# Performance work log

Measured on AMD Instinct MI355X. Metric: run time of the kernel, lower is better.

## Reference

```python
import jax, jax.numpy as jnp
import numpy as np

B, N, H = 2, 4096, 1024
HEADS, DHEAD, M = 16, 64, 256
KERNEL_EPS = 1e-3


def setup_inputs() -> dict:
    key = jax.random.key(0)
    ks = jax.random.split(key, 10)
    w = lambda k, shp: jax.random.normal(k, shp, dtype=jnp.float32) * 0.02
    return {
        "hidden_states": jax.random.normal(ks[0], (B, N, H), dtype=jnp.float32),
        "Wq": w(ks[1], (H, H)), "bq": jnp.zeros((H,), jnp.float32),
        "Wk": w(ks[2], (H, H)), "bk": jnp.zeros((H,), jnp.float32),
        "Wv": w(ks[3], (H, H)), "bv": jnp.zeros((H,), jnp.float32),
        "Wo": w(ks[4], (H, H)), "bo": jnp.zeros((H,), jnp.float32),
        "proj": jax.random.normal(ks[5], (M, DHEAD), dtype=jnp.float32),
    }


def _split_heads(x):
    b, n, _ = x.shape
    return x.reshape(b, n, HEADS, DHEAD).transpose(0, 2, 1, 3)  # [b,h,n,d]


def _softmax_kernel(data, proj, is_query):
    # data: [b,h,n,d]; proj: [m,d]
    data_normalizer = DHEAD ** (-0.25)
    data_dash = jnp.einsum('bhnd,md->bhnm', data_normalizer * data, proj)
    diag_data = -0.5 * jnp.sum(data * data, axis=-1, keepdims=True)  # [b,h,n,1]
    if is_query:
        # argmax over a size-1 last dim -> stabilizer == diag_data itself
        stab = diag_data
    else:
        stab = jnp.max(diag_data)
    kernel_out = jnp.exp(diag_data + (data_dash - stab))  # exp kernel: exp(h + x)
    return (M ** (-0.5)) * (kernel_out + KERNEL_EPS)


def _performer_forward(hidden_states, Wq, bq, Wk, bk, Wv, bv, Wo, bo, proj):
    q = _split_heads(jnp.einsum('bni,oi->bno', hidden_states, Wq) + bq)
    k = _split_heads(jnp.einsum('bni,oi->bno', hidden_states, Wk) + bk)
    v = _split_heads(jnp.einsum('bni,oi->bno', hidden_states, Wv) + bv)

    qf = _softmax_kernel(q, proj, is_query=True)   # [b,h,n,m]
    kf = _softmax_kernel(k, proj, is_query=False)  # [b,h,n,m]

    # linear_attention (non-causal FAVOR+)
    k_cumsum = kf.sum(axis=-2)                                   # [b,h,m]
    d_inv = 1.0 / jnp.einsum('bhnm,bhm->bhn', qf, k_cumsum)      # [b,h,n]
    context = jnp.einsum('bhnm,bhne->bhme', kf, v)               # [b,h,m,d]
    out = jnp.einsum('bhme,bhnm,bhn->bhne', context, qf, d_inv)  # [b,h,n,d]

    out = out.transpose(0, 2, 1, 3).reshape(hidden_states.shape[0], -1, H)
    return jnp.einsum('bni,oi->bno', out, Wo) + bo


def reference(hidden_states, Wq, bq, Wk, bk, Wv, bv, Wo, bo, proj):
    return _performer_forward(hidden_states, Wq, bq, Wk, bk, Wv, bv, Wo, bo, proj)
```

## Files before the change

kernel.cpp:

```cpp
#include <hip/hip_runtime.h>
#include <math.h>

#define B_      2
#define N_      4096
#define H_      1024
#define HEADS_  16
#define DH_     64
#define M_      256
#define NSPLIT  8
#define EPAD    80

constexpr float NORMALIZER = 0.35355339059327373f;
constexpr float RATIO      = 0.0625f;
constexpr float KEPS       = 1e-3f;

typedef __bf16 bf16x8 __attribute__((ext_vector_type(8)));
typedef __bf16 bf16x4 __attribute__((ext_vector_type(4)));
typedef float  f32x4  __attribute__((ext_vector_type(4)));

__global__ __launch_bounds__(256) void split_bf16(
    const float* __restrict__ src, __bf16* __restrict__ hi, __bf16* __restrict__ lo)
{
    int i = blockIdx.x * 256 + threadIdx.x;
    float4 v = ((const float4*)src)[i];
    float vv[4] = {v.x, v.y, v.z, v.w};
    bf16x4 h, l;
#pragma unroll
    for (int j = 0; j < 4; ++j) {
        __bf16 hh = (__bf16)vv[j];
        h[j] = hh;
        l[j] = (__bf16)(vv[j] - (float)hh);
    }
    ((bf16x4*)hi)[i] = h;
    ((bf16x4*)lo)[i] = l;
}

__global__ __launch_bounds__(256) void split_w(
    const float* __restrict__ W0, const float* __restrict__ W1,
    const float* __restrict__ W2, const float* __restrict__ W3,
    __bf16* __restrict__ hi, __bf16* __restrict__ lo)
{
    const float* src = W0;
    if (blockIdx.y == 1) src = W1;
    else if (blockIdx.y == 2) src = W2;
    else if (blockIdx.y == 3) src = W3;
    int i = blockIdx.x * 256 + threadIdx.x;
    size_t o = (size_t)blockIdx.y * 262144 + i;
    float4 v = ((const float4*)src)[i];
    float vv[4] = {v.x, v.y, v.z, v.w};
    bf16x4 h, l;
#pragma unroll
    for (int j = 0; j < 4; ++j) {
        __bf16 hh = (__bf16)vv[j];
        h[j] = hh;
        l[j] = (__bf16)(vv[j] - (float)hh);
    }
    ((bf16x4*)hi)[o] = h;
    ((bf16x4*)lo)[o] = l;
}

__global__ __launch_bounds__(512, 2) void gemm_qkv(
    const __bf16* __restrict__ Ah, const __bf16* __restrict__ Al,
    const __bf16* __restrict__ WH, const __bf16* __restrict__ WL,
    const float* __restrict__ bq, const float* __restrict__ bk, const float* __restrict__ bv,
    __bf16* __restrict__ Qh, __bf16* __restrict__ Ql,
    __bf16* __restrict__ Kh, __bf16* __restrict__ Kl,
    __bf16* __restrict__ Vh, __bf16* __restrict__ Vl)
{
    __shared__ alignas(16) __bf16 lds[2][8][128 * 32];

    const int t    = threadIdx.x;
    const int lane = t & 63;
    const int lm   = lane & 15;
    const int lq   = lane >> 4;
    const int w    = t >> 6;
    const int wm   = (w >> 2) * 64;
    const int wn   = (w & 3) * 32;

    const int wg = blockIdx.x + 8 * blockIdx.y;
    const int sw = (wg & 7) * 64 + (wg >> 3);
    const int n0 = (sw & 7) * 128;
    const int m0 = (sw >> 3) * 128;
    const int K  = 1024;
    const int NK = 32;
    const size_t WSZ = (size_t)H_ * H_;

    const __bf16* mysrc;
    if      (w == 0) mysrc = Ah;
    else if (w == 1) mysrc = Al;
    else             mysrc = ((w & 1) ? WL : WH) + (size_t)((w - 2) >> 1) * WSZ;
    const int rbase  = (w < 2) ? m0 : n0;
    const int rsub   = lane >> 2;
    const int slot   = lane & 3;
    const int schunk = slot ^ ((lane >> 3) & 3);
    const __bf16* gbase = mysrc + (size_t)(rbase + rsub) * K + schunk * 8;

    f32x4 acc[3][4][2];
#pragma unroll
    for (int s = 0; s < 3; ++s)
#pragma unroll
        for (int i = 0; i < 4; ++i)
#pragma unroll
            for (int j = 0; j < 2; ++j) acc[s][i][j] = (f32x4){0.f, 0.f, 0.f, 0.f};

    const int swz = (lq ^ ((lm >> 1) & 3)) * 8;

    auto stage = [&](int buf, int k0) {
#pragma unroll
        for (int c = 0; c < 8; ++c) {
            const __bf16* g = gbase + (size_t)c * 16 * K + k0;
            __builtin_amdgcn_global_load_lds(
                (const __attribute__((address_space(1))) void*)g,
                (__attribute__((address_space(3))) void*)&lds[buf][w][c * 512],
                16, 0, 0);
        }
    };

#define MFMA_S(S) \
    _Pragma("unroll") \
    for (int i = 0; i < 4; ++i) \
        _Pragma("unroll") \
        for (int j = 0; j < 2; ++j) { \
            acc[S][i][j] = __builtin_amdgcn_mfma_f32_16x16x32_bf16(ah[i], bh[j], acc[S][i][j], 0, 0, 0); \
            acc[S][i][j] = __builtin_amdgcn_mfma_f32_16x16x32_bf16(al[i], bh[j], acc[S][i][j], 0, 0, 0); \
            acc[S][i][j] = __builtin_amdgcn_mfma_f32_16x16x32_bf16(ah[i], bl[j], acc[S][i][j], 0, 0, 0); \
        }

    stage(0, 0);
    int p = 0;
#pragma unroll 1
    for (int kt = 0; kt < NK; ++kt) {
        const int nb  = p ^ 1;
        const int nk0 = (kt + 1) * 32;
        const bool more = (kt < NK - 1);
        bf16x8 ah[4], al[4], bh[2], bl[2];

        if (w < 4) asm volatile("s_waitcnt vmcnt(0)" ::: "memory");
        asm volatile("s_barrier" ::: "memory");
#pragma unroll
        for (int i = 0; i < 4; ++i) {
            int off = (wm + i * 16 + lm) * 32 + swz;
            ah[i] = *(const bf16x8*)&lds[p][0][off];
            al[i] = *(const bf16x8*)&lds[p][1][off];
        }
#pragma unroll
        for (int j = 0; j < 2; ++j) {
            int off = (wn + j * 16 + lm) * 32 + swz;
            bh[j] = *(const bf16x8*)&lds[p][2][off];
            bl[j] = *(const bf16x8*)&lds[p][3][off];
        }
        if (more && w < 4) stage(nb, nk0);
        asm volatile("s_waitcnt lgkmcnt(0)" ::: "memory");
        __builtin_amdgcn_sched_barrier(0);
        __builtin_amdgcn_s_setprio(1);
        MFMA_S(0)
        __builtin_amdgcn_s_setprio(0);

        if (w == 4 || w == 5) asm volatile("s_waitcnt vmcnt(0)" ::: "memory");
        asm volatile("s_barrier" ::: "memory");
#pragma unroll
        for (int j = 0; j < 2; ++j) {
            int off = (wn + j * 16 + lm) * 32 + swz;
            bh[j] = *(const bf16x8*)&lds[p][4][off];
            bl[j] = *(const bf16x8*)&lds[p][5][off];
        }
        if (more && (w == 4 || w == 5)) stage(nb, nk0);
        asm volatile("s_waitcnt lgkmcnt(0)" ::: "memory");
        __builtin_amdgcn_sched_barrier(0);
        __builtin_amdgcn_s_setprio(1);
        MFMA_S(1)
        __builtin_amdgcn_s_setprio(0);

        if (w >= 6) asm volatile("s_waitcnt vmcnt(0)" ::: "memory");
        asm volatile("s_barrier" ::: "memory");
#pragma unroll
        for (int j = 0; j < 2; ++j) {
            int off = (wn + j * 16 + lm) * 32 + swz;
            bh[j] = *(const bf16x8*)&lds[p][6][off];
            bl[j] = *(const bf16x8*)&lds[p][7][off];
        }
        if (more && w >= 6) stage(nb, nk0);
        asm volatile("s_waitcnt lgkmcnt(0)" ::: "memory");
        __builtin_amdgcn_sched_barrier(0);
        __builtin_amdgcn_s_setprio(1);
        MFMA_S(2)
        __builtin_amdgcn_s_setprio(0);

        p ^= 1;
    }
#undef MFMA_S

    const float* biases[3] = {bq, bk, bv};
    __bf16* Chs[3] = {Qh, Kh, Vh};
    __bf16* Cls[3] = {Ql, Kl, Vl};
#pragma unroll
    for (int s = 0; s < 3; ++s) {
        float bsr[2];
#pragma unroll
        for (int j = 0; j < 2; ++j) bsr[j] = biases[s][n0 + wn + j * 16 + lm];
#pragma unroll
        for (int i = 0; i < 4; ++i)
#pragma unroll
            for (int r = 0; r < 4; ++r) {
                int rowm = m0 + wm + i * 16 + lq * 4 + r;
#pragma unroll
                for (int j = 0; j < 2; ++j) {
                    int col = n0 + wn + j * 16 + lm;
                    float o = acc[s][i][j][r] + bsr[j];
                    __bf16 hh = (__bf16)o;
                    Chs[s][(size_t)rowm * 1024 + col] = hh;
                    Cls[s][(size_t)rowm * 1024 + col] = (__bf16)(o - (float)hh);
                }
            }
    }
}

__global__ __launch_bounds__(512, 4) void gemm_out(
    const __bf16* __restrict__ Ah, const __bf16* __restrict__ Al,
    const __bf16* __restrict__ Bh, const __bf16* __restrict__ Bl,
    const float* __restrict__ bias, float* __restrict__ C0)
{
    __shared__ alignas(16) __bf16 lds[2][4][128 * 32];

    const int t    = threadIdx.x;
    const int lane = t & 63;
    const int lm   = lane & 15;
    const int lq   = lane >> 4;
    const int w    = t >> 6;
    const int wm   = (w >> 2) * 64;
    const int wn   = (w & 3) * 32;

    const int wg = blockIdx.x + 8 * blockIdx.y;
    const int sw = (wg & 7) * 64 + (wg >> 3);
    const int n0 = (sw & 7) * 128;
    const int m0 = (sw >> 3) * 128;
    const int K  = 1024;
    const int NK = 32;

    const int tw = w >> 1;
    const int hw = w & 1;
    const __bf16* mysrc = (tw == 0) ? Ah : (tw == 1) ? Al : (tw == 2) ? Bh : Bl;
    const int     rbase = ((tw < 2) ? m0 : n0) + hw * 64;
    const int rsub   = lane >> 2;
    const int slot   = lane & 3;
    const int schunk = slot ^ ((lane >> 3) & 3);
    const __bf16* gbase = mysrc + (size_t)(rbase + rsub) * K + schunk * 8;

    f32x4 acc[4][2];
#pragma unroll
    for (int i = 0; i < 4; ++i)
#pragma unroll
        for (int j = 0; j < 2; ++j) acc[i][j] = (f32x4){0.f, 0.f, 0.f, 0.f};

    const int swz = (lq ^ ((lm >> 1) & 3)) * 8;

    auto stage = [&](int buf, int k0) {
#pragma unroll
        for (int c = 0; c < 4; ++c) {
            const __bf16* g = gbase + (size_t)c * 16 * K + k0;
            __builtin_amdgcn_global_load_lds(
                (const __attribute__((address_space(1))) void*)g,
                (__attribute__((address_space(3))) void*)&lds[buf][tw][(hw * 64 + c * 16) * 32],
                16, 0, 0);
        }
    };

    auto compute = [&](int p) {
        const __bf16* tAh = lds[p][0];
        const __bf16* tAl = lds[p][1];
        const __bf16* tBh = lds[p][2];
        const __bf16* tBl = lds[p][3];
        bf16x8 bh[2], bl[2];
#pragma unroll
        for (int j = 0; j < 2; ++j) {
            int off = (wn + j * 16 + lm) * 32 + swz;
            bh[j] = *(const bf16x8*)&tBh[off];
            bl[j] = *(const bf16x8*)&tBl[off];
        }
#pragma unroll
        for (int i = 0; i < 4; ++i) {
            int off = (wm + i * 16 + lm) * 32 + swz;
            bf16x8 ah = *(const bf16x8*)&tAh[off];
            bf16x8 al = *(const bf16x8*)&tAl[off];
#pragma unroll
            for (int j = 0; j < 2; ++j) {
                acc[i][j] = __builtin_amdgcn_mfma_f32_16x16x32_bf16(ah, bh[j], acc[i][j], 0, 0, 0);
                acc[i][j] = __builtin_amdgcn_mfma_f32_16x16x32_bf16(al, bh[j], acc[i][j], 0, 0, 0);
                acc[i][j] = __builtin_amdgcn_mfma_f32_16x16x32_bf16(ah, bl[j], acc[i][j], 0, 0, 0);
            }
        }
    };

    stage(0, 0);
    int p = 0;
#pragma unroll 1
    for (int kk = 0; kk < NK - 1; ++kk) {
        stage(p ^ 1, (kk + 1) * 32);
        asm volatile("s_waitcnt vmcnt(4)" ::: "memory");
        asm volatile("s_barrier" ::: "memory");
        compute(p);
        asm volatile("s_barrier" ::: "memory");
        p ^= 1;
    }
    asm volatile("s_waitcnt vmcnt(0)" ::: "memory");
    asm volatile("s_barrier" ::: "memory");
    compute(p);

    float bsr[2];
#pragma unroll
    for (int j = 0; j < 2; ++j) bsr[j] = bias[n0 + wn + j * 16 + lm];
#pragma unroll
    for (int i = 0; i < 4; ++i)
#pragma unroll
        for (int r = 0; r < 4; ++r) {
            int rowm = m0 + wm + i * 16 + lq * 4 + r;
#pragma unroll
            for (int j = 0; j < 2; ++j) {
                int col = n0 + wn + j * 16 + lm;
                C0[(size_t)rowm * 1024 + col] = acc[i][j][r] + bsr[j];
            }
        }
}

__global__ __launch_bounds__(256) void diag_kernel(
    const __bf16* __restrict__ Kh, const __bf16* __restrict__ Kl,
    float* __restrict__ diag, float* __restrict__ partials)
{
    int gt = blockIdx.x * 256 + threadIdx.x;
    int r  = gt >> 2;
    int q  = gt & 3;
    const bf16x8* ph = (const bf16x8*)(Kh + (size_t)r * 64 + q * 16);
    const bf16x8* pl = (const bf16x8*)(Kl + (size_t)r * 64 + q * 16);
    float s = 0.f;
#pragma unroll
    for (int i = 0; i < 2; ++i) {
        bf16x8 vh = ph[i], vl = pl[i];
#pragma unroll
        for (int j = 0; j < 8; ++j) {
            float x = (float)vh[j] + (float)vl[j];
            s += x * x;
        }
    }
    s += __shfl_xor(s, 1);
    s += __shfl_xor(s, 2);
    float d = -0.5f * s;
    if (q == 0) {
        int h = r & 15, bn = r >> 4;
        int n = bn & 4095, b = bn >> 12;
        diag[(((size_t)b * 16 + h) << 12) + n] = d;
    }
    __shared__ float red[256];
    red[threadIdx.x] = d;
    __syncthreads();
    for (int s2 = 128; s2 > 0; s2 >>= 1) {
        if (threadIdx.x < s2) red[threadIdx.x] = fmaxf(red[threadIdx.x], red[threadIdx.x + s2]);
        __syncthreads();
    }
    if (threadIdx.x == 0) partials[blockIdx.x] = red[0];
}

__global__ __launch_bounds__(256) void reduce_stab(
    const float* __restrict__ partials, float* __restrict__ stab, int n)
{
    float m = -3.0e38f;
    for (int i = threadIdx.x; i < n; i += 256) m = fmaxf(m, partials[i]);
    __shared__ float red[256];
    red[threadIdx.x] = m;
    __syncthreads();
    for (int s2 = 128; s2 > 0; s2 >>= 1) {
        if (threadIdx.x < s2) red[threadIdx.x] = fmaxf(red[threadIdx.x], red[threadIdx.x + s2]);
        __syncthreads();
    }
    if (threadIdx.x == 0) stab[0] = red[0];
}

__global__ __launch_bounds__(256, 2) void ctx_mfma(
    const __bf16* __restrict__ Kh, const __bf16* __restrict__ Kl,
    const __bf16* __restrict__ Vh, const __bf16* __restrict__ Vl,
    const __bf16* __restrict__ projH, const __bf16* __restrict__ projL,
    const float* __restrict__ diag, const float* __restrict__ stabp,
    float* __restrict__ ctxp)
{
    __shared__ alignas(16) char ldsbuf[59904];
    __shared__ float dg[64];
    __bf16* kfTh = (__bf16*)ldsbuf;
    __bf16* kfTl = kfTh + 9216;
    __bf16* vTh  = kfTl + 9216;
    __bf16* vTl  = vTh + 5760;
    float*  ctxe = (float*)ldsbuf;

    const int t    = threadIdx.x;
    const int lane = t & 63;
    const int w    = t >> 6;
    const int lm   = lane & 15;
    const int lq   = lane >> 4;
    const int bh   = blockIdx.z;
    const int b    = bh >> 4, h = bh & 15;
    const int mh   = blockIdx.y;
    const int slice = blockIdx.x;
    const int mwave = mh * 128 + w * 32;
    const float stab = stabp[0];
    const size_t rowbase = (size_t)b * N_ * H_ + (size_t)h * DH_;
    const float* diag_bh = diag + (size_t)bh * N_;

    for (int idx = t; idx < 16 * 72; idx += 256) {
        int e = 64 + idx / 72, n = idx % 72;
        vTh[e * 72 + n] = (e == 64 && n < 64) ? (__bf16)1.0f : (__bf16)0.0f;
        vTl[e * 72 + n] = (__bf16)0.0f;
    }

    bf16x8 ph[2][2], pl[2][2];
#pragma unroll
    for (int mf = 0; mf < 2; ++mf)
#pragma unroll
        for (int ks = 0; ks < 2; ++ks) {
            size_t pa = (size_t)(mwave + mf * 16 + lm) * 64 + ks * 32 + lq * 8;
            ph[mf][ks] = *(const bf16x8*)(projH + pa);
            pl[mf][ks] = *(const bf16x8*)(projL + pa);
        }

    f32x4 acc[2][5];
#pragma unroll
    for (int mf = 0; mf < 2; ++mf)
#pragma unroll
        for (int ef = 0; ef < 5; ++ef) acc[mf][ef] = (f32x4){0.f, 0.f, 0.f, 0.f};

    const int nl = t >> 2, dc = (t & 3) * 16;
    bf16x8 v0, v1, u0, u1;
    bf16x8 kh_p[4][2], kl_p[4][2];
    float dgr = 0.f;
    {
        const int nbase = slice * (N_ / NSPLIT);
        size_t va = rowbase + (size_t)(nbase + nl) * H_ + dc;
        v0 = *(const bf16x8*)(Vh + va);
        v1 = *(const bf16x8*)(Vh + va + 8);
        u0 = *(const bf16x8*)(Vl + va);
        u1 = *(const bf16x8*)(Vl + va + 8);
#pragma unroll
        for (int nf = 0; nf < 4; ++nf)
#pragma unroll
            for (int ks = 0; ks < 2; ++ks) {
                size_t ka = rowbase + (size_t)(nbase + nf * 16 + lm) * H_ + ks * 32 + lq * 8;
                kh_p[nf][ks] = *(const bf16x8*)(Kh + ka);
                kl_p[nf][ks] = *(const bf16x8*)(Kl + ka);
            }
        if (t < 64) dgr = diag_bh[nbase + t];
    }

    for (int tile = 0; tile < 8; ++tile) {
        const int n0 = slice * (N_ / NSPLIT) + tile * 64;
        __syncthreads();

#pragma unroll
        for (int j = 0; j < 8; ++j) {
            vTh[(dc + j) * 72 + nl]     = v0[j];
            vTh[(dc + 8 + j) * 72 + nl] = v1[j];
            vTl[(dc + j) * 72 + nl]     = u0[j];
            vTl[(dc + 8 + j) * 72 + nl] = u1[j];
        }
        if (t < 64) dg[t] = dgr - stab;

        f32x4 dsh[4][2];
#pragma unroll
        for (int nf = 0; nf < 4; ++nf) {
#pragma unroll
            for (int mf = 0; mf < 2; ++mf) dsh[nf][mf] = (f32x4){0.f, 0.f, 0.f, 0.f};
#pragma unroll
            for (int mf = 0; mf < 2; ++mf)
#pragma unroll
                for (int ks = 0; ks < 2; ++ks) {
                    dsh[nf][mf] = __builtin_amdgcn_mfma_f32_16x16x32_bf16(kh_p[nf][ks], ph[mf][ks], dsh[nf][mf], 0, 0, 0);
                    dsh[nf][mf] = __builtin_amdgcn_mfma_f32_16x16x32_bf16(kl_p[nf][ks], ph[mf][ks], dsh[nf][mf], 0, 0, 0);
                    dsh[nf][mf] = __builtin_amdgcn_mfma_f32_16x16x32_bf16(kh_p[nf][ks], pl[mf][ks], dsh[nf][mf], 0, 0, 0);
                }
        }

        __syncthreads();

        if (tile < 7) {
            size_t va = rowbase + (size_t)(n0 + 64 + nl) * H_ + dc;
            v0 = *(const bf16x8*)(Vh + va);
            v1 = *(const bf16x8*)(Vh + va + 8);
            u0 = *(const bf16x8*)(Vl + va);
            u1 = *(const bf16x8*)(Vl + va + 8);
#pragma unroll
            for (int nf = 0; nf < 4; ++nf)
#pragma unroll
                for (int ks = 0; ks < 2; ++ks) {
                    size_t ka = rowbase + (size_t)(n0 + 64 + nf * 16 + lm) * H_ + ks * 32 + lq * 8;
                    kh_p[nf][ks] = *(const bf16x8*)(Kh + ka);
                    kl_p[nf][ks] = *(const bf16x8*)(Kl + ka);
                }
            if (t < 64) dgr = diag_bh[n0 + 64 + t];
        }

#pragma unroll
        for (int nf = 0; nf < 4; ++nf) {
            float4 dgv = *(const float4*)&dg[nf * 16 + lq * 4];
            float dga[4] = {dgv.x, dgv.y, dgv.z, dgv.w};
#pragma unroll
            for (int mf = 0; mf < 2; ++mf) {
                int mrow = w * 32 + mf * 16 + lm;
                bf16x4 vh_, vl_;
#pragma unroll
                for (int r = 0; r < 4; ++r) {
                    float kf = RATIO * (__expf(dga[r] + NORMALIZER * dsh[nf][mf][r]) + KEPS);
                    __bf16 hh = (__bf16)kf;
                    vh_[r] = hh;
                    vl_[r] = (__bf16)(kf - (float)hh);
                }
                int nbase = nf * 16 + lq * 4;
                *(bf16x4*)&kfTh[mrow * 72 + nbase] = vh_;
                *(bf16x4*)&kfTl[mrow * 72 + nbase] = vl_;
            }
        }

#pragma unroll
        for (int ks = 0; ks < 2; ++ks) {
#pragma unroll
            for (int mf = 0; mf < 2; ++mf) {
                bf16x8 af = *(const bf16x8*)&kfTh[(w * 32 + mf * 16 + lm) * 72 + ks * 32 + lq * 8];
                bf16x8 afl = *(const bf16x8*)&kfTl[(w * 32 + mf * 16 + lm) * 72 + ks * 32 + lq * 8];
#pragma unroll
                for (int ef = 0; ef < 5; ++ef) {
                    bf16x8 bfh = *(const bf16x8*)&vTh[(ef * 16 + lm) * 72 + ks * 32 + lq * 8];
                    bf16x8 bfl = *(const bf16x8*)&vTl[(ef * 16 + lm) * 72 + ks * 32 + lq * 8];
                    acc[mf][ef] = __builtin_amdgcn_mfma_f32_16x16x32_bf16(af,  bfh, acc[mf][ef], 0, 0, 0);
                    acc[mf][ef] = __builtin_amdgcn_mfma_f32_16x16x32_bf16(afl, bfh, acc[mf][ef], 0, 0, 0);
                    acc[mf][ef] = __builtin_amdgcn_mfma_f32_16x16x32_bf16(af,  bfl, acc[mf][ef], 0, 0, 0);
                }
            }
        }
    }

    __syncthreads();
#pragma unroll
    for (int mf = 0; mf < 2; ++mf)
#pragma unroll
        for (int ef = 0; ef < 5; ++ef)
#pragma unroll
            for (int r = 0; r < 4; ++r) {
                int ml = w * 32 + mf * 16 + lq * 4 + r;
                int e  = ef * 16 + lm;
                ctxe[ml * 81 + e] = acc[mf][ef][r];
            }
    __syncthreads();
    const size_t SLICE = (size_t)(B_ * HEADS_) * EPAD * M_;
    const size_t obase = (size_t)slice * SLICE + (size_t)bh * EPAD * M_;
    for (int i = t; i < EPAD * 128; i += 256) {
        int e = i >> 7, ml = i & 127;
        ctxp[obase + (size_t)e * M_ + mh * 128 + ml] = ctxe[ml * 81 + e];
    }
}

__global__ __launch_bounds__(256) void ctx_reduce(
    const float* __restrict__ ctxp, __bf16* __restrict__ ctxTh, __bf16* __restrict__ ctxTl)
{
    int idx = blockIdx.x * 256 + threadIdx.x;
    const size_t SLICE = (size_t)(B_ * HEADS_) * EPAD * M_;
    float s = 0.f;
#pragma unroll
    for (int k = 0; k < NSPLIT; ++k) s += ctxp[(size_t)k * SLICE + idx];
    __bf16 hh = (__bf16)s;
    ctxTh[idx] = hh;
    ctxTl[idx] = (__bf16)(s - (float)hh);
}

__global__ __launch_bounds__(512, 2) void out_mfma(
    const __bf16* __restrict__ Qh, const __bf16* __restrict__ Ql,
    const __bf16* __restrict__ projH, const __bf16* __restrict__ projL,
    const __bf16* __restrict__ ctxTh, const __bf16* __restrict__ ctxTl,
    __bf16* __restrict__ attnH, __bf16* __restrict__ attnL)
{
    __shared__ alignas(16) __bf16 ctxLh[80 * 256];
    __shared__ alignas(16) __bf16 ctxLl[80 * 256];
    __shared__ alignas(16) __bf16 qfh[8][32][72];
    __shared__ alignas(16) __bf16 qfl[8][32][72];

    const int t    = threadIdx.x;
    const int lane = t & 63;
    const int w    = t >> 6;
    const int lm   = lane & 15;
    const int lq   = lane >> 4;
    const int bh   = blockIdx.y;
    const int b    = bh >> 4, h = bh & 15;
    const int nw   = blockIdx.x * 256 + w * 32;
    const size_t rowbase = (size_t)b * N_ * H_ + (size_t)h * DH_;

    const __bf16* cth = ctxTh + (size_t)bh * EPAD * M_;
    const __bf16* ctl = ctxTl + (size_t)bh * EPAD * M_;

    {
        const int r_in = lane >> 5;
        const int cp   = lane & 31;
#pragma unroll
        for (int c = 0; c < 5; ++c) {
            int idx = w * 5 + c;
            int r   = idx * 2 + r_in;
            int gc  = cp ^ (r & 7);
            const __bf16* gh = cth + (size_t)r * 256 + gc * 8;
            const __bf16* gl = ctl + (size_t)r * 256 + gc * 8;
            __builtin_amdgcn_global_load_lds(
                (const __attribute__((address_space(1))) void*)gh,
                (__attribute__((address_space(3))) void*)&ctxLh[idx * 512],
                16, 0, 0);
            __builtin_amdgcn_global_load_lds(
                (const __attribute__((address_space(1))) void*)gl,
                (__attribute__((address_space(3))) void*)&ctxLl[idx * 512],
                16, 0, 0);
        }
    }

    bf16x8 qh_[2][2], ql_[2][2];
#pragma unroll
    for (int nf = 0; nf < 2; ++nf)
#pragma unroll
        for (int ks = 0; ks < 2; ++ks) {
            size_t qa = rowbase + (size_t)(nw + nf * 16 + lm) * H_ + ks * 32 + lq * 8;
            qh_[nf][ks] = *(const bf16x8*)(Qh + qa);
            ql_[nf][ks] = *(const bf16x8*)(Ql + qa);
        }
    bf16x8 pc_h[4][2], pc_l[4][2];
#pragma unroll
    for (int mf = 0; mf < 4; ++mf)
#pragma unroll
        for (int ks = 0; ks < 2; ++ks) {
            size_t pa = (size_t)(mf * 16 + lm) * 64 + ks * 32 + lq * 8;
            pc_h[mf][ks] = *(const bf16x8*)(projH + pa);
            pc_l[mf][ks] = *(const bf16x8*)(projL + pa);
        }

    __syncthreads();

    f32x4 accO[2][5];
#pragma unroll
    for (int nf = 0; nf < 2; ++nf)
#pragma unroll
        for (int ef = 0; ef < 5; ++ef) accO[nf][ef] = (f32x4){0.f, 0.f, 0.f, 0.f};

#pragma unroll
    for (int mc = 0; mc < 4; ++mc) {
        const int m0 = mc * 64;
        f32x4 dsh[2][4];
#pragma unroll
        for (int nf = 0; nf < 2; ++nf)
#pragma unroll
            for (int mf = 0; mf < 4; ++mf) dsh[nf][mf] = (f32x4){0.f, 0.f, 0.f, 0.f};
#pragma unroll
        for (int mf = 0; mf < 4; ++mf)
#pragma unroll
            for (int ks = 0; ks < 2; ++ks)
#pragma unroll
                for (int nf = 0; nf < 2; ++nf) {
                    dsh[nf][mf] = __builtin_amdgcn_mfma_f32_16x16x32_bf16(qh_[nf][ks], pc_h[mf][ks], dsh[nf][mf], 0, 0, 0);
                    dsh[nf][mf] = __builtin_amdgcn_mfma_f32_16x16x32_bf16(ql_[nf][ks], pc_h[mf][ks], dsh[nf][mf], 0, 0, 0);
                    dsh[nf][mf] = __builtin_amdgcn_mfma_f32_16x16x32_bf16(qh_[nf][ks], pc_l[mf][ks], dsh[nf][mf], 0, 0, 0);
                }
        bf16x8 pn_h[4][2], pn_l[4][2];
        if (mc < 3) {
#pragma unroll
            for (int mf = 0; mf < 4; ++mf)
#pragma unroll
                for (int ks = 0; ks < 2; ++ks) {
                    size_t pa = (size_t)((m0 + 64) + mf * 16 + lm) * 64 + ks * 32 + lq * 8;
                    pn_h[mf][ks] = *(const bf16x8*)(projH + pa);
                    pn_l[mf][ks] = *(const bf16x8*)(projL + pa);
                }
        }
#pragma unroll
        for (int nf = 0; nf < 2; ++nf)
#pragma unroll
            for (int mf = 0; mf < 4; ++mf)
#pragma unroll
                for (int r = 0; r < 4; ++r) {
                    float qf = RATIO * (__expf(NORMALIZER * dsh[nf][mf][r]) + KEPS);
                    __bf16 hh = (__bf16)qf;
                    int nloc = nf * 16 + lq * 4 + r;
                    qfh[w][nloc][mf * 16 + lm] = hh;
                    qfl[w][nloc][mf * 16 + lm] = (__bf16)(qf - (float)hh);
                }
#pragma unroll
        for (int ks = 0; ks < 2; ++ks) {
            bf16x8 af[2], afl[2];
#pragma unroll
            for (int nf = 0; nf < 2; ++nf) {
                af[nf]  = *(const bf16x8*)&qfh[w][nf * 16 + lm][ks * 32 + lq * 8];
                afl[nf] = *(const bf16x8*)&qfl[w][nf * 16 + lm][ks * 32 + lq * 8];
            }
#pragma unroll
            for (int ef = 0; ef < 5; ++ef) {
                int row = ef * 16 + lm;
                int sc  = ((m0 >> 3) + ks * 4 + lq) ^ (lm & 7);
                int off = row * 256 + sc * 8;
                bf16x8 bfh = *(const bf16x8*)&ctxLh[off];
                bf16x8 bfl = *(const bf16x8*)&ctxLl[off];
#pragma unroll
                for (int nf = 0; nf < 2; ++nf) {
                    accO[nf][ef] = __builtin_amdgcn_mfma_f32_16x16x32_bf16(af[nf],  bfh, accO[nf][ef], 0, 0, 0);
                    accO[nf][ef] = __builtin_amdgcn_mfma_f32_16x16x32_bf16(afl[nf], bfh, accO[nf][ef], 0, 0, 0);
                    accO[nf][ef] = __builtin_amdgcn_mfma_f32_16x16x32_bf16(af[nf],  bfl, accO[nf][ef], 0, 0, 0);
                }
            }
        }
        if (mc < 3) {
#pragma unroll
            for (int mf = 0; mf < 4; ++mf)
#pragma unroll
                for (int ks = 0; ks < 2; ++ks) {
                    pc_h[mf][ks] = pn_h[mf][ks];
                    pc_l[mf][ks] = pn_l[mf][ks];
                }
        }
    }

#pragma unroll
    for (int nf = 0; nf < 2; ++nf) {
        float dinv[4];
#pragma unroll
        for (int r = 0; r < 4; ++r) {
            float den = __shfl(accO[nf][4][r], lane & 48);
            dinv[r] = 1.f / den;
        }
#pragma unroll
        for (int ef = 0; ef < 4; ++ef)
#pragma unroll
            for (int r = 0; r < 4; ++r) {
                float o = accO[nf][ef][r] * dinv[r];
                __bf16 hh = (__bf16)o;
                size_t oa = rowbase + (size_t)(nw + nf * 16 + lq * 4 + r) * H_ + ef * 16 + lm;
                attnH[oa] = hh;
                attnL[oa] = (__bf16)(o - (float)hh);
            }
    }
}

extern "C" void kernel_launch(void* const* d_in, const int* in_sizes, int n_in,
                              void* d_out, int out_size, void* d_ws, size_t ws_size,
                              hipStream_t stream) {
    const float* hs   = (const float*)d_in[0];
    const float* Wq   = (const float*)d_in[1];
    const float* bq   = (const float*)d_in[2];
    const float* Wk   = (const float*)d_in[3];
    const float* bk   = (const float*)d_in[4];
    const float* Wv   = (const float*)d_in[5];
    const float* bv   = (const float*)d_in[6];
    const float* Wo   = (const float*)d_in[7];
    const float* bo   = (const float*)d_in[8];
    const float* proj = (const float*)d_in[9];
    float* out = (float*)d_out;

    const size_t QSZ = (size_t)B_ * N_ * H_;
    const size_t WSZ = (size_t)H_ * H_;
    const size_t CTXT = (size_t)B_ * HEADS_ * EPAD * M_;

    __bf16* Qh  = (__bf16*)d_ws;
    __bf16* Ql  = Qh + QSZ;
    __bf16* Kh  = Ql + QSZ;
    __bf16* Kl  = Kh + QSZ;
    __bf16* Vh  = Kl + QSZ;
    __bf16* Vl  = Vh + QSZ;
    __bf16* hsH = Vl + QSZ;
    __bf16* hsL = hsH + QSZ;
    __bf16* WH  = hsL + QSZ;
    __bf16* WL  = WH + 4 * WSZ;
    __bf16* projH = WL + 4 * WSZ;
    __bf16* projL = projH + (size_t)M_ * DH_;
    __bf16* ctxTh = projL + (size_t)M_ * DH_;
    __bf16* ctxTl = ctxTh + CTXT;
    float*  diag  = (float*)(ctxTl + CTXT);
    float*  parts = diag + (size_t)B_ * HEADS_ * N_;
    float*  stab  = parts + 2048;
    float*  ctxp  = stab + 16;

    __bf16 *WoH = WH + 3*WSZ, *WoL = WL + 3*WSZ;

    split_bf16<<<QSZ / 4 / 256, 256, 0, stream>>>(hs, hsH, hsL);
    split_w<<<dim3(WSZ / 4 / 256, 4), 256, 0, stream>>>(Wq, Wk, Wv, Wo, WH, WL);
    split_bf16<<<(M_ * DH_) / 4 / 256, 256, 0, stream>>>(proj, projH, projL);

    gemm_qkv<<<dim3(H_ / 128, (B_ * N_) / 128), 512, 0, stream>>>(
        hsH, hsL, WH, WL, bq, bk, bv, Qh, Ql, Kh, Kl, Vh, Vl);

    diag_kernel<<<2048, 256, 0, stream>>>(Kh, Kl, diag, parts);
    reduce_stab<<<1, 256, 0, stream>>>(parts, stab, 2048);

    ctx_mfma<<<dim3(NSPLIT, 2, B_ * HEADS_), 256, 0, stream>>>(
        Kh, Kl, Vh, Vl, projH, projL, diag, stab, ctxp);

    ctx_reduce<<<(B_ * HEADS_ * EPAD * M_) / 256, 256, 0, stream>>>(ctxp, ctxTh, ctxTl);

    out_mfma<<<dim3(N_ / 256, B_ * HEADS_), 512, 0, stream>>>(
        Qh, Ql, projH, projL, ctxTh, ctxTl, hsH, hsL);

    gemm_out<<<dim3(H_ / 128, (B_ * N_) / 128), 512, 0, stream>>>(
        hsH, hsL, WoH, WoL, bo, out);
}
```

Baseline: 415.6 us.

## Compute k_cumsum and denominator in FP32 instead of padded ones-column MFMA

Drops the extra 16-wide ones/padding column block that folded k_cumsum and the normalizer into the MFMA context and output GEMMs. k_cumsum is now summed in registers within ctx_mfma, written per slice, reduced in ctx_reduce, and the denominator is formed as an FP32 dot product of qf with kcum in out_mfma. This removes a fifth of the MFMA work and the LDS and global traffic for the padded rows, at the cost of scalar FMAs, shuffles and an extra small reduction buffer.

```diff
diff --git a/kernel.cpp b/kernel.cpp
--- a/kernel.cpp
+++ b/kernel.cpp
@@ -8,7 +8,6 @@
 #define DH_     64
 #define M_      256
 #define NSPLIT  8
-#define EPAD    80
 
 constexpr float NORMALIZER = 0.35355339059327373f;
 constexpr float RATIO      = 0.0625f;
@@ -379,14 +378,14 @@
     const __bf16* __restrict__ Vh, const __bf16* __restrict__ Vl,
     const __bf16* __restrict__ projH, const __bf16* __restrict__ projL,
     const float* __restrict__ diag, const float* __restrict__ stabp,
-    float* __restrict__ ctxp)
+    float* __restrict__ ctxp, float* __restrict__ kcump)
 {
-    __shared__ alignas(16) char ldsbuf[59904];
+    __shared__ alignas(16) char ldsbuf[55296];
     __shared__ float dg[64];
     __bf16* kfTh = (__bf16*)ldsbuf;
     __bf16* kfTl = kfTh + 9216;
     __bf16* vTh  = kfTl + 9216;
-    __bf16* vTl  = vTh + 5760;
+    __bf16* vTl  = vTh + 4608;
     float*  ctxe = (float*)ldsbuf;
 
     const int t    = threadIdx.x;
@@ -403,12 +402,6 @@
     const size_t rowbase = (size_t)b * N_ * H_ + (size_t)h * DH_;
     const float* diag_bh = diag + (size_t)bh * N_;
 
-    for (int idx = t; idx < 16 * 72; idx += 256) {
-        int e = 64 + idx / 72, n = idx % 72;
-        vTh[e * 72 + n] = (e == 64 && n < 64) ? (__bf16)1.0f : (__bf16)0.0f;
-        vTl[e * 72 + n] = (__bf16)0.0f;
-    }
-
     bf16x8 ph[2][2], pl[2][2];
 #pragma unroll
     for (int mf = 0; mf < 2; ++mf)
@@ -419,11 +412,12 @@
             pl[mf][ks] = *(const bf16x8*)(projL + pa);
         }
 
-    f32x4 acc[2][5];
+    f32x4 acc[2][4];
 #pragma unroll
     for (int mf = 0; mf < 2; ++mf)
 #pragma unroll
-        for (int ef = 0; ef < 5; ++ef) acc[mf][ef] = (f32x4){0.f, 0.f, 0.f, 0.f};
+        for (int ef = 0; ef < 4; ++ef) acc[mf][ef] = (f32x4){0.f, 0.f, 0.f, 0.f};
+    float kcum[2] = {0.f, 0.f};
 
     const int nl = t >> 2, dc = (t & 3) * 16;
     bf16x8 v0, v1, u0, u1;
@@ -505,6 +499,7 @@
 #pragma unroll
                 for (int r = 0; r < 4; ++r) {
                     float kf = RATIO * (__expf(dga[r] + NORMALIZER * dsh[nf][mf][r]) + KEPS);
+                    kcum[mf] += kf;
                     __bf16 hh = (__bf16)kf;
                     vh_[r] = hh;
                     vl_[r] = (__bf16)(kf - (float)hh);
@@ -522,7 +517,7 @@
                 bf16x8 af = *(const bf16x8*)&kfTh[(w * 32 + mf * 16 + lm) * 72 + ks * 32 + lq * 8];
                 bf16x8 afl = *(const bf16x8*)&kfTl[(w * 32 + mf * 16 + lm) * 72 + ks * 32 + lq * 8];
 #pragma unroll
-                for (int ef = 0; ef < 5; ++ef) {
+                for (int ef = 0; ef < 4; ++ef) {
                     bf16x8 bfh = *(const bf16x8*)&vTh[(ef * 16 + lm) * 72 + ks * 32 + lq * 8];
                     bf16x8 bfl = *(const bf16x8*)&vTl[(ef * 16 + lm) * 72 + ks * 32 + lq * 8];
                     acc[mf][ef] = __builtin_amdgcn_mfma_f32_16x16x32_bf16(af,  bfh, acc[mf][ef], 0, 0, 0);
@@ -533,47 +528,69 @@
         }
     }
 
+#pragma unroll
+    for (int mf = 0; mf < 2; ++mf) {
+        kcum[mf] += __shfl_xor(kcum[mf], 16);
+        kcum[mf] += __shfl_xor(kcum[mf], 32);
+    }
+    if (lq == 0) {
+#pragma unroll
+        for (int mf = 0; mf < 2; ++mf)
+            kcump[(size_t)slice * 8192 + (size_t)bh * 256 + mwave + mf * 16 + lm] = kcum[mf];
+    }
+
     __syncthreads();
 #pragma unroll
     for (int mf = 0; mf < 2; ++mf)
 #pragma unroll
-        for (int ef = 0; ef < 5; ++ef)
+        for (int ef = 0; ef < 4; ++ef)
 #pragma unroll
             for (int r = 0; r < 4; ++r) {
                 int ml = w * 32 + mf * 16 + lq * 4 + r;
                 int e  = ef * 16 + lm;
-                ctxe[ml * 81 + e] = acc[mf][ef][r];
+                ctxe[ml * 65 + e] = acc[mf][ef][r];
             }
     __syncthreads();
-    const size_t SLICE = (size_t)(B_ * HEADS_) * EPAD * M_;
-    const size_t obase = (size_t)slice * SLICE + (size_t)bh * EPAD * M_;
-    for (int i = t; i < EPAD * 128; i += 256) {
+    const size_t SLICE = (size_t)(B_ * HEADS_) * 64 * M_;
+    const size_t obase = (size_t)slice * SLICE + (size_t)bh * 64 * M_;
+    for (int i = t; i < 64 * 128; i += 256) {
         int e = i >> 7, ml = i & 127;
-        ctxp[obase + (size_t)e * M_ + mh * 128 + ml] = ctxe[ml * 81 + e];
+        ctxp[obase + (size_t)e * M_ + mh * 128 + ml] = ctxe[ml * 65 + e];
     }
 }
 
 __global__ __launch_bounds__(256) void ctx_reduce(
-    const float* __restrict__ ctxp, __bf16* __restrict__ ctxTh, __bf16* __restrict__ ctxTl)
+    const float* __restrict__ ctxp, const float* __restrict__ kcump,
+    __bf16* __restrict__ ctxTh, __bf16* __restrict__ ctxTl, float* __restrict__ kcumT)
 {
-    int idx = blockIdx.x * 256 + threadIdx.x;
-    const size_t SLICE = (size_t)(B_ * HEADS_) * EPAD * M_;
-    float s = 0.f;
-#pragma unroll
-    for (int k = 0; k < NSPLIT; ++k) s += ctxp[(size_t)k * SLICE + idx];
-    __bf16 hh = (__bf16)s;
-    ctxTh[idx] = hh;
-    ctxTl[idx] = (__bf16)(s - (float)hh);
+    const int bid = blockIdx.x;
+    if (bid < 2048) {
+        int idx = bid * 256 + threadIdx.x;
+        const size_t SLICE = (size_t)(B_ * HEADS_) * 64 * M_;
+        float s = 0.f;
+#pragma unroll
+        for (int k = 0; k < NSPLIT; ++k) s += ctxp[(size_t)k * SLICE + idx];
+        __bf16 hh = (__bf16)s;
+        ctxTh[idx] = hh;
+        ctxTl[idx] = (__bf16)(s - (float)hh);
+    } else {
+        int idx = (bid - 2048) * 256 + threadIdx.x;
+        float s = 0.f;
+#pragma unroll
+        for (int k = 0; k < NSPLIT; ++k) s += kcump[(size_t)k * 8192 + idx];
+        kcumT[idx] = s;
+    }
 }
 
 __global__ __launch_bounds__(512, 2) void out_mfma(
     const __bf16* __restrict__ Qh, const __bf16* __restrict__ Ql,
     const __bf16* __restrict__ projH, const __bf16* __restrict__ projL,
     const __bf16* __restrict__ ctxTh, const __bf16* __restrict__ ctxTl,
+    const float* __restrict__ kcumT,
     __bf16* __restrict__ attnH, __bf16* __restrict__ attnL)
 {
-    __shared__ alignas(16) __bf16 ctxLh[80 * 256];
-    __shared__ alignas(16) __bf16 ctxLl[80 * 256];
+    __shared__ alignas(16) __bf16 ctxLh[64 * 256];
+    __shared__ alignas(16) __bf16 ctxLl[64 * 256];
     __shared__ alignas(16) __bf16 qfh[8][32][72];
     __shared__ alignas(16) __bf16 qfl[8][32][72];
 
@@ -587,15 +604,16 @@
     const int nw   = blockIdx.x * 256 + w * 32;
     const size_t rowbase = (size_t)b * N_ * H_ + (size_t)h * DH_;
 
-    const __bf16* cth = ctxTh + (size_t)bh * EPAD * M_;
-    const __bf16* ctl = ctxTl + (size_t)bh * EPAD * M_;
+    const __bf16* cth = ctxTh + (size_t)bh * 64 * M_;
+    const __bf16* ctl = ctxTl + (size_t)bh * 64 * M_;
+    const float*  kct = kcumT + (size_t)bh * M_;
 
     {
         const int r_in = lane >> 5;
         const int cp   = lane & 31;
 #pragma unroll
-        for (int c = 0; c < 5; ++c) {
-            int idx = w * 5 + c;
+        for (int c = 0; c < 4; ++c) {
+            int idx = w * 4 + c;
             int r   = idx * 2 + r_in;
             int gc  = cp ^ (r & 7);
             const __bf16* gh = cth + (size_t)r * 256 + gc * 8;
@@ -632,15 +650,23 @@
 
     __syncthreads();
 
-    f32x4 accO[2][5];
+    f32x4 accO[2][4];
 #pragma unroll
     for (int nf = 0; nf < 2; ++nf)
 #pragma unroll
-        for (int ef = 0; ef < 5; ++ef) accO[nf][ef] = (f32x4){0.f, 0.f, 0.f, 0.f};
+        for (int ef = 0; ef < 4; ++ef) accO[nf][ef] = (f32x4){0.f, 0.f, 0.f, 0.f};
+    float den_p[2][4];
+#pragma unroll
+    for (int nf = 0; nf < 2; ++nf)
+#pragma unroll
+        for (int r = 0; r < 4; ++r) den_p[nf][r] = 0.f;
 
 #pragma unroll
     for (int mc = 0; mc < 4; ++mc) {
         const int m0 = mc * 64;
+        float kc[4];
+#pragma unroll
+        for (int mf = 0; mf < 4; ++mf) kc[mf] = kct[m0 + mf * 16 + lm];
         f32x4 dsh[2][4];
 #pragma unroll
         for (int nf = 0; nf < 2; ++nf)
@@ -674,6 +700,7 @@
 #pragma unroll
                 for (int r = 0; r < 4; ++r) {
                     float qf = RATIO * (__expf(NORMALIZER * dsh[nf][mf][r]) + KEPS);
+                    den_p[nf][r] += qf * kc[mf];
                     __bf16 hh = (__bf16)qf;
                     int nloc = nf * 16 + lq * 4 + r;
                     qfh[w][nloc][mf * 16 + lm] = hh;
@@ -688,7 +715,7 @@
                 afl[nf] = *(const bf16x8*)&qfl[w][nf * 16 + lm][ks * 32 + lq * 8];
             }
 #pragma unroll
-            for (int ef = 0; ef < 5; ++ef) {
+            for (int ef = 0; ef < 4; ++ef) {
                 int row = ef * 16 + lm;
                 int sc  = ((m0 >> 3) + ks * 4 + lq) ^ (lm & 7);
                 int off = row * 256 + sc * 8;
@@ -714,24 +741,29 @@
     }
 
 #pragma unroll
-    for (int nf = 0; nf < 2; ++nf) {
-        float dinv[4];
+    for (int nf = 0; nf < 2; ++nf)
 #pragma unroll
         for (int r = 0; r < 4; ++r) {
-            float den = __shfl(accO[nf][4][r], lane & 48);
-            dinv[r] = 1.f / den;
-        }
+            float d = den_p[nf][r];
+            d += __shfl_xor(d, 1);
+            d += __shfl_xor(d, 2);
+            d += __shfl_xor(d, 4);
+            d += __shfl_xor(d, 8);
+            den_p[nf][r] = 1.f / d;
+        }
+
+#pragma unroll
+    for (int nf = 0; nf < 2; ++nf)
 #pragma unroll
         for (int ef = 0; ef < 4; ++ef)
 #pragma unroll
             for (int r = 0; r < 4; ++r) {
-                float o = accO[nf][ef][r] * dinv[r];
+                float o = accO[nf][ef][r] * den_p[nf][r];
                 __bf16 hh = (__bf16)o;
                 size_t oa = rowbase + (size_t)(nw + nf * 16 + lq * 4 + r) * H_ + ef * 16 + lm;
                 attnH[oa] = hh;
                 attnL[oa] = (__bf16)(o - (float)hh);
             }
-    }
 }
 
 extern "C" void kernel_launch(void* const* d_in, const int* in_sizes, int n_in,
@@ -751,7 +783,7 @@
 
     const size_t QSZ = (size_t)B_ * N_ * H_;
     const size_t WSZ = (size_t)H_ * H_;
-    const size_t CTXT = (size_t)B_ * HEADS_ * EPAD * M_;
+    const size_t CTXT = (size_t)B_ * HEADS_ * 64 * M_;
 
     __bf16* Qh  = (__bf16*)d_ws;
     __bf16* Ql  = Qh + QSZ;
@@ -767,10 +799,12 @@
     __bf16* projL = projH + (size_t)M_ * DH_;
     __bf16* ctxTh = projL + (size_t)M_ * DH_;
     __bf16* ctxTl = ctxTh + CTXT;
-    float*  diag  = (float*)(ctxTl + CTXT);
+    float*  kcumT = (float*)(ctxTl + CTXT);
+    float*  diag  = kcumT + 8192;
     float*  parts = diag + (size_t)B_ * HEADS_ * N_;
     float*  stab  = parts + 2048;
     float*  ctxp  = stab + 16;
+    float*  kcump = ctxp + (size_t)NSPLIT * CTXT;
 
     __bf16 *WoH = WH + 3*WSZ, *WoL = WL + 3*WSZ;
 
@@ -785,12 +819,12 @@
     reduce_stab<<<1, 256, 0, stream>>>(parts, stab, 2048);
 
     ctx_mfma<<<dim3(NSPLIT, 2, B_ * HEADS_), 256, 0, stream>>>(
-        Kh, Kl, Vh, Vl, projH, projL, diag, stab, ctxp);
-
-    ctx_reduce<<<(B_ * HEADS_ * EPAD * M_) / 256, 256, 0, stream>>>(ctxp, ctxTh, ctxTl);
+        Kh, Kl, Vh, Vl, projH, projL, diag, stab, ctxp, kcump);
+
+    ctx_reduce<<<2048 + 32, 256, 0, stream>>>(ctxp, kcump, ctxTh, ctxTl, kcumT);
 
     out_mfma<<<dim3(N_ / 256, B_ * HEADS_), 512, 0, stream>>>(
-        Qh, Ql, projH, projL, ctxTh, ctxTl, hsH, hsL);
+        Qh, Ql, projH, projL, ctxTh, ctxTl, kcumT, hsH, hsL);
 
     gemm_out<<<dim3(H_ / 128, (B_ * N_) / 128), 512, 0, stream>>>(
         hsH, hsL, WoH, WoL, bo, out);
```

New measurement: 434.8 us. 4.6% more time.
